# Performance work log

Measured on AMD Instinct MI355X. Metric: run time of the kernel, lower is better.

Reference implementation:

```python
import jax, jax.numpy as jnp
import numpy as np

N_HEADS = 12


def setup_inputs() -> dict:
    key = jax.random.key(0)
    ks = jax.random.split(key, 4)
    B, T, C = 1, 4096, 768
    x = jax.random.normal(ks[0], (B, T, C), dtype=jnp.float32)
    w_qkv = jax.random.normal(ks[1], (C, 3 * C), dtype=jnp.float32) * (C ** -0.5)
    b_qkv = jnp.zeros((3 * C,), dtype=jnp.float32)
    w_proj = jax.random.normal(ks[2], (C, C), dtype=jnp.float32) * (C ** -0.5)
    b_proj = jnp.zeros((C,), dtype=jnp.float32)
    return {"x": x, "w_qkv": w_qkv, "b_qkv": b_qkv, "w_proj": w_proj, "b_proj": b_proj}


def reference(x, w_qkv, b_qkv, w_proj, b_proj):
    B, T, C = x.shape
    H = N_HEADS
    hd = C // H
    qkv = x @ w_qkv + b_qkv                      # [B,T,3C]
    q, k, v = jnp.split(qkv, 3, axis=-1)
    # [B,H,T,hd]
    q = q.reshape(B, T, H, hd).transpose(0, 2, 1, 3)
    k = k.reshape(B, T, H, hd).transpose(0, 2, 1, 3)
    v = v.reshape(B, T, H, hd).transpose(0, 2, 1, 3)
    scale = 1.0 / jnp.sqrt(jnp.float32(hd))
    attn = jnp.einsum('bhqd,bhkd->bhqk', q, k) * scale  # [B,H,T,T]
    causal = jnp.tril(jnp.ones((T, T), dtype=bool))
    attn = jnp.where(causal, attn, jnp.float32(-jnp.inf))
    attn = jax.nn.softmax(attn, axis=-1)
    out = jnp.einsum('bhqk,bhkd->bhqd', attn, v)        # [B,H,T,hd]
    out = out.transpose(0, 2, 1, 3).reshape(B, T, C)
    return out @ w_proj + b_proj
```

## Files before the change

### kernel.cpp

```cpp
#include <hip/hip_runtime.h>
#include <hip/hip_bf16.h>


#define T_SEQ 4096
#define C_DIM 768
#define C3    2304
#define NH    12
#define HD    64

typedef __attribute__((ext_vector_type(8))) short bf16x8;
typedef __attribute__((ext_vector_type(4))) short bf16x4;
typedef __attribute__((ext_vector_type(4))) float f32x4;

__device__ inline unsigned short f2bf(float f) {
  union { float f; unsigned u; } v; v.f = f;
  unsigned r = v.u + 0x7fff + ((v.u >> 16) & 1);
  return (unsigned short)(r >> 16);
}
__device__ inline unsigned short f2bf_trunc(float f) {
  union { float f; unsigned u; } v; v.f = f;
  return (unsigned short)(v.u >> 16);
}

__device__ inline void gl2lds16(const void* g, void* l) {
  __builtin_amdgcn_global_load_lds(
      (const __attribute__((address_space(1))) unsigned int*)g,
      (__attribute__((address_space(3))) unsigned int*)l, 16, 0, 0);
}

#if __has_builtin(__builtin_amdgcn_exp2f)
#define EXP2F(x) __builtin_amdgcn_exp2f(x)
#else
#define EXP2F(x) exp2f(x)
#endif

#define NB_CONV  (T_SEQ * C_DIM / 2048)
#define NB_TQKV  ((C3 / 32) * (C_DIM / 32))
#define NB_TPROJ ((C_DIM / 32) * (C_DIM / 32))

__global__ __launch_bounds__(256) void prep_fused(
    const float* __restrict__ x, const float* __restrict__ w_qkv,
    const float* __restrict__ w_proj, unsigned short* __restrict__ xb,
    unsigned short* __restrict__ wqkvT, unsigned short* __restrict__ wprojT) {
  __shared__ float t[32][33];
  const int b = blockIdx.x;
  const int tid = threadIdx.x;

  if (b < NB_CONV) {
    int i = (b * 256 + tid) * 8;
    float4 v0 = *(const float4*)(x + i);
    float4 v1 = *(const float4*)(x + i + 4);
    unsigned short o[8] = {f2bf(v0.x), f2bf(v0.y), f2bf(v0.z), f2bf(v0.w),
                           f2bf(v1.x), f2bf(v1.y), f2bf(v1.z), f2bf(v1.w)};
    *(uint4*)(xb + i) = *(uint4*)o;
    return;
  }
  const float* in;
  unsigned short* outT;
  int R, Cc, bi;
  if (b < NB_CONV + NB_TQKV) {
    in = w_qkv; outT = wqkvT; R = C_DIM; Cc = C3; bi = b - NB_CONV;
  } else {
    in = w_proj; outT = wprojT; R = C_DIM; Cc = C_DIM; bi = b - NB_CONV - NB_TQKV;
  }
  const int tx = tid & 31, ty = tid >> 5;
  const int c0 = (bi % (Cc / 32)) * 32, r0 = (bi / (Cc / 32)) * 32;
#pragma unroll
  for (int i = 0; i < 4; ++i) {
    int r = ty + i * 8;
    t[r][tx] = in[(size_t)(r0 + r) * Cc + c0 + tx];
  }
  __syncthreads();
#pragma unroll
  for (int i = 0; i < 4; ++i) {
    int c = ty + i * 8;
    outT[(size_t)(c0 + c) * R + r0 + tx] = f2bf(t[tx][c]);
  }
}

__global__ __launch_bounds__(256) void gemm_qkv(
    const unsigned short* __restrict__ A, const unsigned short* __restrict__ Bt,
    const float* __restrict__ bias, unsigned short* __restrict__ Cq,
    unsigned short* __restrict__ vTp, int M, int N, int K) {
  __shared__ unsigned short As[128 * 64];
  __shared__ unsigned short Bs[128 * 64];
  const int tid = threadIdx.x;
  const int wave = tid >> 6, lane = tid & 63;
  const int lo = lane & 15, g8 = lane >> 4;
  const int lo7 = lo & 7;
  const int wm = wave >> 1, wn = wave & 1;
  const int bm = blockIdx.y * 128, bn = blockIdx.x * 128;
  const int drow8 = lane >> 3;
  const int dslot = (lane & 7) * 8;
  const int dsrc = ((lane & 7) ^ drow8) * 8;

  f32x4 acc[4][4];
#pragma unroll
  for (int mt = 0; mt < 4; ++mt)
#pragma unroll
    for (int nt = 0; nt < 4; ++nt) acc[mt][nt] = (f32x4){0.f, 0.f, 0.f, 0.f};

  const unsigned short* Abase = A + (size_t)bm * K;
  const unsigned short* Bbase = Bt + (size_t)bn * K;

  for (int k0 = 0; k0 < K; k0 += 64) {
    __syncthreads();
#pragma unroll
    for (int p = 0; p < 4; ++p) {
      const int r = p * 32 + wave * 8 + drow8;
      gl2lds16(Abase + (size_t)r * K + k0 + dsrc, As + r * 64 + dslot);
      gl2lds16(Bbase + (size_t)r * K + k0 + dsrc, Bs + r * 64 + dslot);
    }
    __syncthreads();

#pragma unroll
    for (int kk = 0; kk < 2; ++kk) {
      bf16x8 a[4], b[4];
#pragma unroll
      for (int mt = 0; mt < 4; ++mt)
        a[mt] = *(const bf16x8*)(
            As + (wm * 64 + mt * 16 + lo) * 64 + (((kk * 4 + g8) ^ lo7) * 8));
#pragma unroll
      for (int nt = 0; nt < 4; ++nt)
        b[nt] = *(const bf16x8*)(
            Bs + (wn * 64 + nt * 16 + lo) * 64 + (((kk * 4 + g8) ^ lo7) * 8));
#pragma unroll
      for (int mt = 0; mt < 4; ++mt)
#pragma unroll
        for (int nt = 0; nt < 4; ++nt)
          acc[mt][nt] = __builtin_amdgcn_mfma_f32_16x16x32_bf16(a[mt], b[nt], acc[mt][nt], 0, 0, 0);
    }
  }

  if (bn < 2 * C_DIM) {
#pragma unroll
    for (int nt = 0; nt < 4; ++nt) {
      const int n = bn + wn * 64 + nt * 16 + lo;
      const float bv = bias[n];
#pragma unroll
      for (int mt = 0; mt < 4; ++mt)
#pragma unroll
        for (int r = 0; r < 4; ++r) {
          const int m = bm + wm * 64 + mt * 16 + g8 * 4 + r;
          Cq[(size_t)m * C3 + n] = f2bf(acc[mt][nt][r] + bv);
        }
    }
  } else {
#pragma unroll
    for (int nt = 0; nt < 4; ++nt) {
      const int n = bn + wn * 64 + nt * 16 + lo;
      const float bv = bias[n];
      unsigned short* row = vTp + (size_t)(n - 2 * C_DIM) * T_SEQ;
#pragma unroll
      for (int mt = 0; mt < 4; ++mt) {
        const int mbase = (bm + wm * 64 + mt * 16 + g8 * 4) & ~31;
        bf16x4 o4;
#pragma unroll
        for (int r = 0; r < 4; ++r) o4[r] = (short)f2bf(acc[mt][nt][r] + bv);
        *(bf16x4*)(row + mbase + 8 * g8 + 4 * (mt & 1)) = o4;
      }
    }
  }
}

__global__ __launch_bounds__(256) void gemm_bt_mfma(
    const unsigned short* __restrict__ A, const unsigned short* __restrict__ Bt,
    const float* __restrict__ bias, float* __restrict__ C,
    int M, int N, int K) {
  __shared__ unsigned short As[128 * 64];
  __shared__ unsigned short Bs[128 * 64];
  const int tid = threadIdx.x;
  const int wave = tid >> 6, lane = tid & 63;
  const int lo = lane & 15, g8 = lane >> 4;
  const int lo7 = lo & 7;
  const int wm = wave >> 1, wn = wave & 1;
  const int bm = blockIdx.y * 128, bn = blockIdx.x * 128;
  const int drow8 = lane >> 3;
  const int dslot = (lane & 7) * 8;
  const int dsrc = ((lane & 7) ^ drow8) * 8;

  f32x4 acc[4][4];
#pragma unroll
  for (int mt = 0; mt < 4; ++mt)
#pragma unroll
    for (int nt = 0; nt < 4; ++nt) acc[mt][nt] = (f32x4){0.f, 0.f, 0.f, 0.f};

  const unsigned short* Abase = A + (size_t)bm * K;
  const unsigned short* Bbase = Bt + (size_t)bn * K;

  for (int k0 = 0; k0 < K; k0 += 64) {
    __syncthreads();
#pragma unroll
    for (int p = 0; p < 4; ++p) {
      const int r = p * 32 + wave * 8 + drow8;
      gl2lds16(Abase + (size_t)r * K + k0 + dsrc, As + r * 64 + dslot);
      gl2lds16(Bbase + (size_t)r * K + k0 + dsrc, Bs + r * 64 + dslot);
    }
    __syncthreads();

#pragma unroll
    for (int kk = 0; kk < 2; ++kk) {
      bf16x8 a[4], b[4];
#pragma unroll
      for (int mt = 0; mt < 4; ++mt)
        a[mt] = *(const bf16x8*)(
            As + (wm * 64 + mt * 16 + lo) * 64 + (((kk * 4 + g8) ^ lo7) * 8));
#pragma unroll
      for (int nt = 0; nt < 4; ++nt)
        b[nt] = *(const bf16x8*)(
            Bs + (wn * 64 + nt * 16 + lo) * 64 + (((kk * 4 + g8) ^ lo7) * 8));
#pragma unroll
      for (int mt = 0; mt < 4; ++mt)
#pragma unroll
        for (int nt = 0; nt < 4; ++nt)
          acc[mt][nt] = __builtin_amdgcn_mfma_f32_16x16x32_bf16(a[mt], b[nt], acc[mt][nt], 0, 0, 0);
    }
  }

#pragma unroll
  for (int nt = 0; nt < 4; ++nt) {
    const int n = bn + wn * 64 + nt * 16 + lo;
    const float bv = bias[n];
#pragma unroll
    for (int mt = 0; mt < 4; ++mt)
#pragma unroll
      for (int r = 0; r < 4; ++r) {
        const int m = bm + wm * 64 + mt * 16 + g8 * 4 + r;
        C[(size_t)m * N + n] = acc[mt][nt][r] + bv;
      }
  }
}

__global__ __launch_bounds__(256) void flash_attn_mfma13(
    const unsigned short* __restrict__ qkv,
    const unsigned short* __restrict__ vTp,
    unsigned short* __restrict__ out) {
  __shared__ unsigned short Ks[3][64 * 64];
  __shared__ unsigned short Vs[3][64 * 64];

  const int bid = blockIdx.x;
  const int xcd = bid & 7;
  const int j = bid >> 3;
  const int slot = j >> 5;
  const int cc = j & 31;
  const int Hh = 3 * xcd + slot;
  const int h = Hh >> 1;
  const int par = Hh & 1;
  const int qi = (slot == 0) ? cc : (slot == 1) ? (31 - cc) : (cc ^ 16);
  const int qt = 2 * qi + par;
  const int q0 = qt * 64;

  const int tid = threadIdx.x;
  const int w = tid >> 6;
  const int lane = tid & 63;
  const int lo = lane & 15;
  const int g = lane >> 4;
  const int lo7 = lo & 7;
  const float qscale = 0.125f * 1.44269504f;

  const unsigned short* Kg = qkv + C_DIM + h * HD;
  const unsigned short* Vg = vTp + (size_t)(h * HD) * T_SEQ;

  const int drow = tid >> 3;
  const int dslot = (tid & 7) * 8;
  const int dsrc = ((tid & 7) ^ (drow & 7)) * 8;

  bf16x8 qb[2];
#pragma unroll
  for (int dh = 0; dh < 2; ++dh)
    qb[dh] = *(const bf16x8*)(
        qkv + (size_t)(q0 + w * 16 + lo) * C3 + h * HD + dh * 32 + g * 8);

#pragma unroll
  for (int p2 = 0; p2 < 2; ++p2) {
    const int r = p2 * 32 + drow;
    gl2lds16(Kg + (size_t)r * C3 + dsrc, Ks[0] + r * 64 + dslot);
    gl2lds16(Vg + (size_t)r * T_SEQ + dsrc, Vs[0] + r * 64 + dslot);
  }
  if (qt >= 1) {
#pragma unroll
    for (int p2 = 0; p2 < 2; ++p2) {
      const int r = p2 * 32 + drow;
      gl2lds16(Kg + (size_t)(64 + r) * C3 + dsrc, Ks[1] + r * 64 + dslot);
      gl2lds16(Vg + (size_t)r * T_SEQ + 64 + dsrc, Vs[1] + r * 64 + dslot);
    }
    asm volatile("s_waitcnt vmcnt(4)" ::: "memory");
  } else {
    asm volatile("s_waitcnt vmcnt(0)" ::: "memory");
  }
  __builtin_amdgcn_s_barrier();

  float l_i = 0.f;
  f32x4 o_acc[4];
#pragma unroll
  for (int dt = 0; dt < 4; ++dt) o_acc[dt] = (f32x4){0.f, 0.f, 0.f, 0.f};

  int ic = 0;
  int iw = 2;
  for (int t = 0; t <= qt; ++t) {
    if (t + 2 <= qt) {
      const int k0n = (t + 2) * 64;
      unsigned short* Kd = Ks[iw];
      unsigned short* Vd = Vs[iw];
#pragma unroll
      for (int p2 = 0; p2 < 2; ++p2) {
        const int r = p2 * 32 + drow;
        gl2lds16(Kg + (size_t)(k0n + r) * C3 + dsrc, Kd + r * 64 + dslot);
        gl2lds16(Vg + (size_t)r * T_SEQ + k0n + dsrc, Vd + r * 64 + dslot);
      }
    }
    const unsigned short* Kc = Ks[ic];
    const unsigned short* Vc = Vs[ic];

    f32x4 st[4];
#pragma unroll
    for (int mt = 0; mt < 4; ++mt) st[mt] = (f32x4){0.f, 0.f, 0.f, 0.f};
#pragma unroll
    for (int mt = 0; mt < 4; ++mt)
#pragma unroll
      for (int dh = 0; dh < 2; ++dh) {
        bf16x8 a = *(const bf16x8*)(
            Kc + (mt * 16 + lo) * 64 + (((dh * 4 + g) ^ lo7) * 8));
        st[mt] = __builtin_amdgcn_mfma_f32_16x16x32_bf16(a, qb[dh], st[mt], 0, 0, 0);
      }

    if (t == qt) {
      const int qloc = w * 16 + lo;
#pragma unroll
      for (int mt = 0; mt < 4; ++mt)
#pragma unroll
        for (int r = 0; r < 4; ++r)
          if (mt * 16 + g * 4 + r > qloc) st[mt][r] = -1e30f;
    }

    float lsum = 0.f;
    bf16x8 pt[2];
#pragma unroll
    for (int kh = 0; kh < 2; ++kh) {
#pragma unroll
      for (int jj = 0; jj < 4; ++jj) {
        float e0 = EXP2F(st[kh * 2][jj] * qscale);
        float e1 = EXP2F(st[kh * 2 + 1][jj] * qscale);
        lsum += e0 + e1;
        pt[kh][jj] = (short)f2bf_trunc(e0);
        pt[kh][4 + jj] = (short)f2bf_trunc(e1);
      }
    }
    l_i += lsum;

#pragma unroll
    for (int dt = 0; dt < 4; ++dt)
#pragma unroll
      for (int kh = 0; kh < 2; ++kh) {
        bf16x8 av = *(const bf16x8*)(
            Vc + (dt * 16 + lo) * 64 + (((kh * 4 + g) ^ lo7) * 8));
        o_acc[dt] = __builtin_amdgcn_mfma_f32_16x16x32_bf16(av, pt[kh], o_acc[dt], 0, 0, 0);
      }

    if (t + 2 <= qt)
      asm volatile("s_waitcnt vmcnt(4)" ::: "memory");
    else
      asm volatile("s_waitcnt vmcnt(0)" ::: "memory");
    __builtin_amdgcn_s_barrier();

    ic = (ic == 2) ? 0 : ic + 1;
    iw = (iw == 2) ? 0 : iw + 1;
  }

  l_i += __shfl_xor(l_i, 16);
  l_i += __shfl_xor(l_i, 32);
  const float inv = 1.0f / l_i;
  unsigned short* Es = Ks[0];
#pragma unroll
  for (int dt = 0; dt < 4; ++dt) {
    const int chunk = (dt * 2 + (g >> 1)) ^ lo7;
#pragma unroll
    for (int r = 0; r < 4; ++r)
      Es[(w * 16 + lo) * 64 + chunk * 8 + (g & 1) * 4 + r] =
          f2bf(o_acc[dt][r] * inv);
  }
#pragma unroll
  for (int i = 0; i < 2; ++i) {
    const int row = w * 16 + i * 8 + (lane >> 3);
    bf16x8 val = *(const bf16x8*)(Es + row * 64 + (((lane & 7) ^ (row & 7)) * 8));
    *(bf16x8*)(out + (size_t)(q0 + row) * C_DIM + h * HD + (lane & 7) * 8) = val;
  }
}

extern "C" void kernel_launch(void* const* d_in, const int* in_sizes, int n_in,
                              void* d_out, int out_size, void* d_ws, size_t ws_size,
                              hipStream_t stream) {
  const float* x      = (const float*)d_in[0];
  const float* w_qkv  = (const float*)d_in[1];
  const float* b_qkv  = (const float*)d_in[2];
  const float* w_proj = (const float*)d_in[3];
  const float* b_proj = (const float*)d_in[4];
  float* out = (float*)d_out;

  unsigned short* xb     = (unsigned short*)d_ws;
  unsigned short* wqkvT  = xb + (size_t)T_SEQ * C_DIM;
  unsigned short* wprojT = wqkvT + (size_t)C3 * C_DIM;
  unsigned short* qkv    = wprojT + (size_t)C_DIM * C_DIM;
  unsigned short* vTp    = qkv + (size_t)T_SEQ * C3;
  unsigned short* attnb  = vTp + (size_t)C_DIM * T_SEQ;

  prep_fused<<<NB_CONV + NB_TQKV + NB_TPROJ, 256, 0, stream>>>(
      x, w_qkv, w_proj, xb, wqkvT, wprojT);

  gemm_qkv<<<dim3(C3 / 128, T_SEQ / 128), 256, 0, stream>>>(
      xb, wqkvT, b_qkv, qkv, vTp, T_SEQ, C3, C_DIM);

  flash_attn_mfma13<<<T_SEQ / 64 * NH, 256, 0, stream>>>(qkv, vTp, attnb);

  gemm_bt_mfma<<<dim3(C_DIM / 128, T_SEQ / 128), 256, 0, stream>>>(
      attnb, wprojT, b_proj, out, T_SEQ, C_DIM, C_DIM);
}
```

Measured before the change: 188.4 us.

## Balance causal attention work by pairing query tiles with split-KV partials

Each attention block now processes a fixed total of 33 KV tiles. It does this by pairing a long query tile j=63-i (split in two halves across blocks) with a short query tile i. Unnormalized fp32 partial outputs and row sums go to workspace, and a new combine kernel sums them, normalizes, and writes bf16. The goal is to remove the load imbalance of causal attention, where block runtimes varied widely. The cost is an extra kernel launch plus fp32 partial traffic, which relies on softmax without a running max staying consistent across splits.

```diff
diff --git a/kernel.cpp b/kernel.cpp
--- a/kernel.cpp
+++ b/kernel.cpp
@@ -231,24 +231,28 @@
   }
 }
 
-__global__ __launch_bounds__(256) void flash_attn_mfma13(
+#define PO_SLOT ((size_t)NH * 64 * 4096)
+#define PL_SLOT ((size_t)NH * 64 * 64)
+
+__global__ __launch_bounds__(256) void flash_attn_split14(
     const unsigned short* __restrict__ qkv,
     const unsigned short* __restrict__ vTp,
-    unsigned short* __restrict__ out) {
+    float* __restrict__ Po, float* __restrict__ Pl) {
   __shared__ unsigned short Ks[3][64 * 64];
   __shared__ unsigned short Vs[3][64 * 64];
 
   const int bid = blockIdx.x;
   const int xcd = bid & 7;
-  const int j = bid >> 3;
-  const int slot = j >> 5;
-  const int cc = j & 31;
-  const int Hh = 3 * xcd + slot;
+  const int j2 = bid >> 3;
+  const int Hh = xcd * 3 + (j2 >> 5);
   const int h = Hh >> 1;
-  const int par = Hh & 1;
-  const int qi = (slot == 0) ? cc : (slot == 1) ? (31 - cc) : (cc ^ 16);
-  const int qt = 2 * qi + par;
-  const int q0 = qt * 64;
+  const int s = Hh & 1;
+  const int i = j2 & 31;
+  const int j = 63 - i;
+  const int nJ = s ? (31 - i) : 33;
+  const int kJ0 = s ? 33 : 0;
+  const int nI = s ? (i + 1) : 0;
+  const int T = nJ + nI;
 
   const int tid = threadIdx.x;
   const int w = tid >> 6;
@@ -265,30 +269,35 @@
   const int dslot = (tid & 7) * 8;
   const int dsrc = ((tid & 7) ^ (drow & 7)) * 8;
 
-  bf16x8 qb[2];
+  bf16x8 qbJ[2], qbI[2];
 #pragma unroll
   for (int dh = 0; dh < 2; ++dh)
-    qb[dh] = *(const bf16x8*)(
-        qkv + (size_t)(q0 + w * 16 + lo) * C3 + h * HD + dh * 32 + g * 8);
-
-#pragma unroll
-  for (int p2 = 0; p2 < 2; ++p2) {
-    const int r = p2 * 32 + drow;
-    gl2lds16(Kg + (size_t)r * C3 + dsrc, Ks[0] + r * 64 + dslot);
-    gl2lds16(Vg + (size_t)r * T_SEQ + dsrc, Vs[0] + r * 64 + dslot);
-  }
-  if (qt >= 1) {
+    qbJ[dh] = *(const bf16x8*)(
+        qkv + (size_t)(j * 64 + w * 16 + lo) * C3 + h * HD + dh * 32 + g * 8);
+#pragma unroll
+  for (int dh = 0; dh < 2; ++dh)
+    qbI[dh] = *(const bf16x8*)(
+        qkv + (size_t)(i * 64 + w * 16 + lo) * C3 + h * HD + dh * 32 + g * 8);
+
+  auto KT = [&](int t) { return t < nJ ? kJ0 + t : t - nJ; };
+
+  {
+    const int ka = KT(0), kb = KT(1);
 #pragma unroll
     for (int p2 = 0; p2 < 2; ++p2) {
       const int r = p2 * 32 + drow;
-      gl2lds16(Kg + (size_t)(64 + r) * C3 + dsrc, Ks[1] + r * 64 + dslot);
-      gl2lds16(Vg + (size_t)r * T_SEQ + 64 + dsrc, Vs[1] + r * 64 + dslot);
+      gl2lds16(Kg + (size_t)(ka * 64 + r) * C3 + dsrc, Ks[0] + r * 64 + dslot);
+      gl2lds16(Vg + (size_t)r * T_SEQ + ka * 64 + dsrc, Vs[0] + r * 64 + dslot);
+    }
+#pragma unroll
+    for (int p2 = 0; p2 < 2; ++p2) {
+      const int r = p2 * 32 + drow;
+      gl2lds16(Kg + (size_t)(kb * 64 + r) * C3 + dsrc, Ks[1] + r * 64 + dslot);
+      gl2lds16(Vg + (size_t)r * T_SEQ + kb * 64 + dsrc, Vs[1] + r * 64 + dslot);
     }
     asm volatile("s_waitcnt vmcnt(4)" ::: "memory");
-  } else {
-    asm volatile("s_waitcnt vmcnt(0)" ::: "memory");
-  }
-  __builtin_amdgcn_s_barrier();
+    __builtin_amdgcn_s_barrier();
+  }
 
   float l_i = 0.f;
   f32x4 o_acc[4];
@@ -297,20 +306,23 @@
 
   int ic = 0;
   int iw = 2;
-  for (int t = 0; t <= qt; ++t) {
-    if (t + 2 <= qt) {
-      const int k0n = (t + 2) * 64;
+  int t = 0;
+
+  auto body = [&](const bf16x8 (&qb)[2], int qtcur) __attribute__((always_inline)) {
+    if (t + 2 < T) {
+      const int k2 = KT(t + 2);
       unsigned short* Kd = Ks[iw];
       unsigned short* Vd = Vs[iw];
 #pragma unroll
       for (int p2 = 0; p2 < 2; ++p2) {
         const int r = p2 * 32 + drow;
-        gl2lds16(Kg + (size_t)(k0n + r) * C3 + dsrc, Kd + r * 64 + dslot);
-        gl2lds16(Vg + (size_t)r * T_SEQ + k0n + dsrc, Vd + r * 64 + dslot);
+        gl2lds16(Kg + (size_t)(k2 * 64 + r) * C3 + dsrc, Kd + r * 64 + dslot);
+        gl2lds16(Vg + (size_t)r * T_SEQ + k2 * 64 + dsrc, Vd + r * 64 + dslot);
       }
     }
     const unsigned short* Kc = Ks[ic];
     const unsigned short* Vc = Vs[ic];
+    const int ktc = KT(t);
 
     f32x4 st[4];
 #pragma unroll
@@ -324,7 +336,7 @@
         st[mt] = __builtin_amdgcn_mfma_f32_16x16x32_bf16(a, qb[dh], st[mt], 0, 0, 0);
       }
 
-    if (t == qt) {
+    if (ktc == qtcur) {
       const int qloc = w * 16 + lo;
 #pragma unroll
       for (int mt = 0; mt < 4; ++mt)
@@ -357,7 +369,7 @@
         o_acc[dt] = __builtin_amdgcn_mfma_f32_16x16x32_bf16(av, pt[kh], o_acc[dt], 0, 0, 0);
       }
 
-    if (t + 2 <= qt)
+    if (t + 2 < T)
       asm volatile("s_waitcnt vmcnt(4)" ::: "memory");
     else
       asm volatile("s_waitcnt vmcnt(0)" ::: "memory");
@@ -365,26 +377,58 @@
 
     ic = (ic == 2) ? 0 : ic + 1;
     iw = (iw == 2) ? 0 : iw + 1;
-  }
-
-  l_i += __shfl_xor(l_i, 16);
-  l_i += __shfl_xor(l_i, 32);
-  const float inv = 1.0f / l_i;
-  unsigned short* Es = Ks[0];
-#pragma unroll
-  for (int dt = 0; dt < 4; ++dt) {
-    const int chunk = (dt * 2 + (g >> 1)) ^ lo7;
-#pragma unroll
-    for (int r = 0; r < 4; ++r)
-      Es[(w * 16 + lo) * 64 + chunk * 8 + (g & 1) * 4 + r] =
-          f2bf(o_acc[dt][r] * inv);
-  }
-#pragma unroll
-  for (int i = 0; i < 2; ++i) {
-    const int row = w * 16 + i * 8 + (lane >> 3);
-    bf16x8 val = *(const bf16x8*)(Es + row * 64 + (((lane & 7) ^ (row & 7)) * 8));
-    *(bf16x8*)(out + (size_t)(q0 + row) * C_DIM + h * HD + (lane & 7) * 8) = val;
-  }
+    ++t;
+  };
+
+  auto flush = [&](int slot, int qt) __attribute__((always_inline)) {
+    float lred = l_i + __shfl_xor(l_i, 16);
+    lred += __shfl_xor(lred, 32);
+    float* PoS = Po + ((size_t)slot * NH + h) * (64 * 4096) + (size_t)qt * 4096;
+#pragma unroll
+    for (int dt = 0; dt < 4; ++dt)
+      *(f32x4*)(PoS + (w * 16 + lo) * 64 + dt * 16 + g * 4) = o_acc[dt];
+    if (g == 0)
+      Pl[(((size_t)slot * NH + h) * 64 + qt) * 64 + w * 16 + lo] = lred;
+    l_i = 0.f;
+#pragma unroll
+    for (int dt = 0; dt < 4; ++dt) o_acc[dt] = (f32x4){0.f, 0.f, 0.f, 0.f};
+  };
+
+  for (int u = 0; u < nJ; ++u) body(qbJ, j);
+  if (nJ > 0) flush(s, j);
+  for (int u = 0; u < nI; ++u) body(qbI, i);
+  if (nI > 0) flush(0, i);
+}
+
+__global__ __launch_bounds__(256) void combine_partials(
+    const float* __restrict__ Po, const float* __restrict__ Pl,
+    unsigned short* __restrict__ out) {
+  const int bid = blockIdx.x;
+  const int h = bid / 64, qt = bid % 64;
+  const int tid = threadIdx.x;
+  const int q = tid >> 2;
+  const int c = (tid & 3) * 16;
+  const bool two = (qt >= 33);
+  const size_t sl = (size_t)h * 64 + qt;
+  const float* P0 = Po + sl * 4096 + q * 64 + c;
+  const float* P1 = P0 + PO_SLOT;
+  float l = Pl[sl * 64 + q];
+  if (two) l += Pl[PL_SLOT + sl * 64 + q];
+  const float inv = 1.0f / l;
+  unsigned short ob[16];
+#pragma unroll
+  for (int e = 0; e < 4; ++e) {
+    f32x4 v = *(const f32x4*)(P0 + e * 4);
+    if (two) {
+      f32x4 v1 = *(const f32x4*)(P1 + e * 4);
+      v += v1;
+    }
+#pragma unroll
+    for (int r = 0; r < 4; ++r) ob[e * 4 + r] = f2bf(v[r] * inv);
+  }
+  unsigned short* o = out + (size_t)(qt * 64 + q) * C_DIM + h * 64 + c;
+  *(uint4*)o = *(uint4*)ob;
+  *(uint4*)(o + 8) = *(uint4*)(ob + 8);
 }
 
 extern "C" void kernel_launch(void* const* d_in, const int* in_sizes, int n_in,
@@ -403,6 +447,8 @@
   unsigned short* qkv    = wprojT + (size_t)C_DIM * C_DIM;
   unsigned short* vTp    = qkv + (size_t)T_SEQ * C3;
   unsigned short* attnb  = vTp + (size_t)C_DIM * T_SEQ;
+  float* Po = (float*)(attnb + (size_t)T_SEQ * C_DIM);
+  float* Pl = Po + 2 * PO_SLOT;
 
   prep_fused<<<NB_CONV + NB_TQKV + NB_TPROJ, 256, 0, stream>>>(
       x, w_qkv, w_proj, xb, wqkvT, wprojT);
@@ -410,7 +456,9 @@
   gemm_qkv<<<dim3(C3 / 128, T_SEQ / 128), 256, 0, stream>>>(
       xb, wqkvT, b_qkv, qkv, vTp, T_SEQ, C3, C_DIM);
 
-  flash_attn_mfma13<<<T_SEQ / 64 * NH, 256, 0, stream>>>(qkv, vTp, attnb);
+  flash_attn_split14<<<T_SEQ / 64 * NH, 256, 0, stream>>>(qkv, vTp, Po, Pl);
+
+  combine_partials<<<NH * 64, 256, 0, stream>>>(Po, Pl, attnb);
 
   gemm_bt_mfma<<<dim3(C_DIM / 128, T_SEQ / 128), 256, 0, stream>>>(
       attnb, wprojT, b_proj, out, T_SEQ, C_DIM, C_DIM);
```

After: 180.6 us. 4.1% less time.

## Split-K flash attention with 128-row query tiles and combine kernel

Applied to the files above, without the earlier changes.

The attention kernel now processes 128-query tiles per block, so each K/V tile loaded into LDS is reused across twice as many queries. The causal key range is split into up to three chunks, giving 756 balanced blocks with an explicit XCD mapping. Partial outputs and row sums go to fp32 workspace and a new combine kernel reduces and normalizes them. The softmax scale is folded into Q in the QKV GEMM epilogue, row sums are computed with MFMA against a ones vector, and setprio hints are added around MFMA sections. The cost is an extra launch and fp32 partial-result traffic through global memory.

```diff
diff --git a/kernel.cpp b/kernel.cpp
--- a/kernel.cpp
+++ b/kernel.cpp
@@ -133,6 +133,7 @@
   }
 
   if (bn < 2 * C_DIM) {
+    const float sc = (bn < C_DIM) ? 0.18033688011112042f : 1.0f;
 #pragma unroll
     for (int nt = 0; nt < 4; ++nt) {
       const int n = bn + wn * 64 + nt * 16 + lo;
@@ -142,7 +143,7 @@
 #pragma unroll
         for (int r = 0; r < 4; ++r) {
           const int m = bm + wm * 64 + mt * 16 + g8 * 4 + r;
-          Cq[(size_t)m * C3 + n] = f2bf(acc[mt][nt][r] + bv);
+          Cq[(size_t)m * C3 + n] = f2bf((acc[mt][nt][r] + bv) * sc);
         }
     }
   } else {
@@ -231,24 +232,32 @@
   }
 }
 
-__global__ __launch_bounds__(256) void flash_attn_mfma13(
+#define PO_SLOT ((size_t)NH * 32 * 128 * 64)
+#define PL_SLOT ((size_t)NH * 32 * 128)
+#define KSTEP   (64 * C3)
+
+__global__ __launch_bounds__(256) void flash_attn_qb128(
     const unsigned short* __restrict__ qkv,
     const unsigned short* __restrict__ vTp,
-    unsigned short* __restrict__ out) {
+    float* __restrict__ Po, float* __restrict__ Pl) {
   __shared__ unsigned short Ks[3][64 * 64];
   __shared__ unsigned short Vs[3][64 * 64];
 
-  const int bid = blockIdx.x;
-  const int xcd = bid & 7;
-  const int j = bid >> 3;
-  const int slot = j >> 5;
-  const int cc = j & 31;
-  const int Hh = 3 * xcd + slot;
-  const int h = Hh >> 1;
-  const int par = Hh & 1;
-  const int qi = (slot == 0) ? cc : (slot == 1) ? (31 - cc) : (cc ^ 16);
-  const int qt = 2 * qi + par;
-  const int q0 = qt * 64;
+  const int orig = blockIdx.x;
+  const int xcd = orig & 7;
+  const int o8 = orig >> 3;
+  const int idx = ((xcd < 4) ? xcd * 95 : 380 + (xcd - 4) * 94) + o8;
+  const int h = idx / 63;
+  const int rem = idx - h * 63;
+  int qt, c;
+  if (rem < 30)      { qt = 22 + rem / 3;  c = rem % 3; }
+  else if (rem < 52) { int r2 = rem - 30; qt = 11 + (r2 >> 1); c = r2 & 1; }
+  else               { qt = rem - 52;      c = 0; }
+  const int qt2 = 2 * qt;
+  const int k0 = 22 * c;
+  const int kmax = qt2 + 2;
+  const int k1 = (k0 + 22 < kmax) ? (k0 + 22) : kmax;
+  const int T = k1 - k0;
 
   const int tid = threadIdx.x;
   const int w = tid >> 6;
@@ -256,7 +265,6 @@
   const int lo = lane & 15;
   const int g = lane >> 4;
   const int lo7 = lo & 7;
-  const float qscale = 0.125f * 1.44269504f;
 
   const unsigned short* Kg = qkv + C_DIM + h * HD;
   const unsigned short* Vg = vTp + (size_t)(h * HD) * T_SEQ;
@@ -265,99 +273,118 @@
   const int dslot = (tid & 7) * 8;
   const int dsrc = ((tid & 7) ^ (drow & 7)) * 8;
 
-  bf16x8 qb[2];
-#pragma unroll
-  for (int dh = 0; dh < 2; ++dh)
-    qb[dh] = *(const bf16x8*)(
-        qkv + (size_t)(q0 + w * 16 + lo) * C3 + h * HD + dh * 32 + g * 8);
-
-#pragma unroll
-  for (int p2 = 0; p2 < 2; ++p2) {
-    const int r = p2 * 32 + drow;
-    gl2lds16(Kg + (size_t)r * C3 + dsrc, Ks[0] + r * 64 + dslot);
-    gl2lds16(Vg + (size_t)r * T_SEQ + dsrc, Vs[0] + r * 64 + dslot);
-  }
-  if (qt >= 1) {
-#pragma unroll
-    for (int p2 = 0; p2 < 2; ++p2) {
-      const int r = p2 * 32 + drow;
-      gl2lds16(Kg + (size_t)(64 + r) * C3 + dsrc, Ks[1] + r * 64 + dslot);
-      gl2lds16(Vg + (size_t)r * T_SEQ + 64 + dsrc, Vs[1] + r * 64 + dslot);
-    }
-    asm volatile("s_waitcnt vmcnt(4)" ::: "memory");
-  } else {
-    asm volatile("s_waitcnt vmcnt(0)" ::: "memory");
-  }
+  const int qw0 = w * 32 + lo;
+  bf16x8 qb[2][2];
+#pragma unroll
+  for (int qh = 0; qh < 2; ++qh)
+#pragma unroll
+    for (int dh = 0; dh < 2; ++dh)
+      qb[qh][dh] = *(const bf16x8*)(
+          qkv + (size_t)(qt * 128 + qw0 + qh * 16) * C3 + h * HD + dh * 32 + g * 8);
+
+  const unsigned short* pK0 = Kg + (size_t)k0 * KSTEP + (size_t)drow * C3 + dsrc;
+  const unsigned short* pK1 = pK0 + (size_t)32 * C3;
+  const unsigned short* pV0 = Vg + (size_t)drow * T_SEQ + k0 * 64 + dsrc;
+  const unsigned short* pV1 = pV0 + (size_t)32 * T_SEQ;
+
+  auto stage = [&](int buf) __attribute__((always_inline)) {
+    gl2lds16(pK0, Ks[buf] + drow * 64 + dslot);
+    gl2lds16(pK1, Ks[buf] + (32 + drow) * 64 + dslot);
+    gl2lds16(pV0, Vs[buf] + drow * 64 + dslot);
+    gl2lds16(pV1, Vs[buf] + (32 + drow) * 64 + dslot);
+    pK0 += KSTEP; pK1 += KSTEP; pV0 += 64; pV1 += 64;
+  };
+
+  bf16x8 onesb;
+#pragma unroll
+  for (int e = 0; e < 8; ++e) onesb[e] = (short)0x3F80;
+
+  stage(0);
+  stage(1);
+  asm volatile("s_waitcnt vmcnt(4)" ::: "memory");
   __builtin_amdgcn_s_barrier();
 
-  float l_i = 0.f;
-  f32x4 o_acc[4];
-#pragma unroll
-  for (int dt = 0; dt < 4; ++dt) o_acc[dt] = (f32x4){0.f, 0.f, 0.f, 0.f};
-
-  int ic = 0;
-  int iw = 2;
-  for (int t = 0; t <= qt; ++t) {
-    if (t + 2 <= qt) {
-      const int k0n = (t + 2) * 64;
-      unsigned short* Kd = Ks[iw];
-      unsigned short* Vd = Vs[iw];
-#pragma unroll
-      for (int p2 = 0; p2 < 2; ++p2) {
-        const int r = p2 * 32 + drow;
-        gl2lds16(Kg + (size_t)(k0n + r) * C3 + dsrc, Kd + r * 64 + dslot);
-        gl2lds16(Vg + (size_t)r * T_SEQ + k0n + dsrc, Vd + r * 64 + dslot);
-      }
-    }
+  f32x4 o_acc[2][4];
+  f32x4 lacc[2];
+#pragma unroll
+  for (int qh = 0; qh < 2; ++qh) {
+    lacc[qh] = (f32x4){0.f, 0.f, 0.f, 0.f};
+#pragma unroll
+    for (int dt = 0; dt < 4; ++dt) o_acc[qh][dt] = (f32x4){0.f, 0.f, 0.f, 0.f};
+  }
+
+  int ic = 0, iw = 2;
+  int ktc = k0;
+  for (int t = 0; t < T; ++t) {
+    if (t + 2 < T) stage(iw);
     const unsigned short* Kc = Ks[ic];
     const unsigned short* Vc = Vs[ic];
 
-    f32x4 st[4];
-#pragma unroll
-    for (int mt = 0; mt < 4; ++mt) st[mt] = (f32x4){0.f, 0.f, 0.f, 0.f};
+    f32x4 st[2][4];
+#pragma unroll
+    for (int qh = 0; qh < 2; ++qh)
+#pragma unroll
+      for (int mt = 0; mt < 4; ++mt) st[qh][mt] = (f32x4){0.f, 0.f, 0.f, 0.f};
+    __builtin_amdgcn_s_setprio(1);
 #pragma unroll
     for (int mt = 0; mt < 4; ++mt)
 #pragma unroll
       for (int dh = 0; dh < 2; ++dh) {
         bf16x8 a = *(const bf16x8*)(
             Kc + (mt * 16 + lo) * 64 + (((dh * 4 + g) ^ lo7) * 8));
-        st[mt] = __builtin_amdgcn_mfma_f32_16x16x32_bf16(a, qb[dh], st[mt], 0, 0, 0);
+#pragma unroll
+        for (int qh = 0; qh < 2; ++qh)
+          st[qh][mt] = __builtin_amdgcn_mfma_f32_16x16x32_bf16(
+              a, qb[qh][dh], st[qh][mt], 0, 0, 0);
       }
-
-    if (t == qt) {
-      const int qloc = w * 16 + lo;
-#pragma unroll
-      for (int mt = 0; mt < 4; ++mt)
-#pragma unroll
-        for (int r = 0; r < 4; ++r)
-          if (mt * 16 + g * 4 + r > qloc) st[mt][r] = -1e30f;
-    }
-
-    float lsum = 0.f;
-    bf16x8 pt[2];
-#pragma unroll
-    for (int kh = 0; kh < 2; ++kh) {
-#pragma unroll
-      for (int jj = 0; jj < 4; ++jj) {
-        float e0 = EXP2F(st[kh * 2][jj] * qscale);
-        float e1 = EXP2F(st[kh * 2 + 1][jj] * qscale);
-        lsum += e0 + e1;
-        pt[kh][jj] = (short)f2bf_trunc(e0);
-        pt[kh][4 + jj] = (short)f2bf_trunc(e1);
+    __builtin_amdgcn_s_setprio(0);
+
+    if (ktc >= qt2) {
+      const int mb = (ktc == qt2) ? 0 : 64;
+#pragma unroll
+      for (int qh = 0; qh < 2; ++qh) {
+        const int qr = qw0 + qh * 16;
+#pragma unroll
+        for (int mt = 0; mt < 4; ++mt)
+#pragma unroll
+          for (int r = 0; r < 4; ++r)
+            if (mb + mt * 16 + g * 4 + r > qr) st[qh][mt][r] = -1e30f;
       }
     }
-    l_i += lsum;
-
+
+    bf16x8 pt[2][2];
+#pragma unroll
+    for (int qh = 0; qh < 2; ++qh)
+#pragma unroll
+      for (int kh = 0; kh < 2; ++kh)
+#pragma unroll
+        for (int jj = 0; jj < 4; ++jj) {
+          float e0 = EXP2F(st[qh][kh * 2][jj]);
+          float e1 = EXP2F(st[qh][kh * 2 + 1][jj]);
+          pt[qh][kh][jj] = (short)f2bf_trunc(e0);
+          pt[qh][kh][4 + jj] = (short)f2bf_trunc(e1);
+        }
+
+    __builtin_amdgcn_s_setprio(1);
+#pragma unroll
+    for (int qh = 0; qh < 2; ++qh) {
+      lacc[qh] = __builtin_amdgcn_mfma_f32_16x16x32_bf16(onesb, pt[qh][0], lacc[qh], 0, 0, 0);
+      lacc[qh] = __builtin_amdgcn_mfma_f32_16x16x32_bf16(onesb, pt[qh][1], lacc[qh], 0, 0, 0);
+    }
 #pragma unroll
     for (int dt = 0; dt < 4; ++dt)
 #pragma unroll
       for (int kh = 0; kh < 2; ++kh) {
         bf16x8 av = *(const bf16x8*)(
             Vc + (dt * 16 + lo) * 64 + (((kh * 4 + g) ^ lo7) * 8));
-        o_acc[dt] = __builtin_amdgcn_mfma_f32_16x16x32_bf16(av, pt[kh], o_acc[dt], 0, 0, 0);
+#pragma unroll
+        for (int qh = 0; qh < 2; ++qh)
+          o_acc[qh][dt] = __builtin_amdgcn_mfma_f32_16x16x32_bf16(
+              av, pt[qh][kh], o_acc[qh][dt], 0, 0, 0);
       }
-
-    if (t + 2 <= qt)
+    __builtin_amdgcn_s_setprio(0);
+
+    if (t + 2 < T)
       asm volatile("s_waitcnt vmcnt(4)" ::: "memory");
     else
       asm volatile("s_waitcnt vmcnt(0)" ::: "memory");
@@ -365,26 +392,51 @@
 
     ic = (ic == 2) ? 0 : ic + 1;
     iw = (iw == 2) ? 0 : iw + 1;
-  }
-
-  l_i += __shfl_xor(l_i, 16);
-  l_i += __shfl_xor(l_i, 32);
-  const float inv = 1.0f / l_i;
-  unsigned short* Es = Ks[0];
-#pragma unroll
-  for (int dt = 0; dt < 4; ++dt) {
-    const int chunk = (dt * 2 + (g >> 1)) ^ lo7;
-#pragma unroll
-    for (int r = 0; r < 4; ++r)
-      Es[(w * 16 + lo) * 64 + chunk * 8 + (g & 1) * 4 + r] =
-          f2bf(o_acc[dt][r] * inv);
-  }
-#pragma unroll
-  for (int i = 0; i < 2; ++i) {
-    const int row = w * 16 + i * 8 + (lane >> 3);
-    bf16x8 val = *(const bf16x8*)(Es + row * 64 + (((lane & 7) ^ (row & 7)) * 8));
-    *(bf16x8*)(out + (size_t)(q0 + row) * C_DIM + h * HD + (lane & 7) * 8) = val;
-  }
+    ++ktc;
+  }
+
+  float* PoS = Po + (((size_t)c * NH + h) * 32 + qt) * (128 * 64);
+#pragma unroll
+  for (int qh = 0; qh < 2; ++qh)
+#pragma unroll
+    for (int dt = 0; dt < 4; ++dt)
+      *(f32x4*)(PoS + (qw0 + qh * 16) * 64 + dt * 16 + g * 4) = o_acc[qh][dt];
+  if (g == 0) {
+    float* PlS = Pl + (((size_t)c * NH + h) * 32 + qt) * 128;
+#pragma unroll
+    for (int qh = 0; qh < 2; ++qh) PlS[qw0 + qh * 16] = lacc[qh][0];
+  }
+}
+
+__global__ __launch_bounds__(256) void combine_qb128(
+    const float* __restrict__ Po, const float* __restrict__ Pl,
+    unsigned short* __restrict__ out) {
+  const int bid = blockIdx.x;
+  const int h = bid >> 5, qt = bid & 31;
+  const int tid = threadIdx.x;
+  const int q = tid >> 1;
+  const int c0 = (tid & 1) * 32;
+  const bool v1 = (qt >= 11);
+  const bool v2 = (qt >= 22);
+  const size_t base = (size_t)h * 32 + qt;
+  const float* P0 = Po + base * (128 * 64) + q * 64 + c0;
+  float l = Pl[base * 128 + q];
+  if (v1) l += Pl[PL_SLOT + base * 128 + q];
+  if (v2) l += Pl[2 * PL_SLOT + base * 128 + q];
+  const float inv = 1.0f / l;
+  unsigned short ob[32];
+#pragma unroll
+  for (int e = 0; e < 8; ++e) {
+    f32x4 v = *(const f32x4*)(P0 + e * 4);
+    if (v1) v += *(const f32x4*)(P0 + PO_SLOT + e * 4);
+    if (v2) v += *(const f32x4*)(P0 + 2 * PO_SLOT + e * 4);
+#pragma unroll
+    for (int r = 0; r < 4; ++r) ob[e * 4 + r] = f2bf(v[r] * inv);
+  }
+  unsigned short* op = out + (size_t)(qt * 128 + q) * C_DIM + h * 64 + c0;
+#pragma unroll
+  for (int e2 = 0; e2 < 4; ++e2)
+    *(uint4*)(op + e2 * 8) = *(uint4*)(ob + e2 * 8);
 }
 
 extern "C" void kernel_launch(void* const* d_in, const int* in_sizes, int n_in,
@@ -403,6 +455,8 @@
   unsigned short* qkv    = wprojT + (size_t)C_DIM * C_DIM;
   unsigned short* vTp    = qkv + (size_t)T_SEQ * C3;
   unsigned short* attnb  = vTp + (size_t)C_DIM * T_SEQ;
+  float* Po = (float*)(attnb + (size_t)T_SEQ * C_DIM);
+  float* Pl = Po + 3 * PO_SLOT;
 
   prep_fused<<<NB_CONV + NB_TQKV + NB_TPROJ, 256, 0, stream>>>(
       x, w_qkv, w_proj, xb, wqkvT, wprojT);
@@ -410,7 +464,9 @@
   gemm_qkv<<<dim3(C3 / 128, T_SEQ / 128), 256, 0, stream>>>(
       xb, wqkvT, b_qkv, qkv, vTp, T_SEQ, C3, C_DIM);
 
-  flash_attn_mfma13<<<T_SEQ / 64 * NH, 256, 0, stream>>>(qkv, vTp, attnb);
+  flash_attn_qb128<<<756, 256, 0, stream>>>(qkv, vTp, Po, Pl);
+
+  combine_qb128<<<NH * 32, 256, 0, stream>>>(Po, Pl, attnb);
 
   gemm_bt_mfma<<<dim3(C_DIM / 128, T_SEQ / 128), 256, 0, stream>>>(
       attnb, wprojT, b_proj, out, T_SEQ, C_DIM, C_DIM);
```

Result: no change. 187.2 us (-0.6%).
